# Optimization experiments

Hardware: AMD Instinct MI355X
Metric: run time of the kernel (lower is better)

## Reference

```python
import jax, jax.numpy as jnp
import numpy as np

HEADS = 4
N_NODES = 100000
N_EDGES = 800000
N_LAB = 200000
IN_CH = 64
HID = 32
OUT_CH = 32
EXPR_OUT = 500


def _gat_conv(x, edge_index, W, a_src, a_dst, bias, out_per_head):
    """PyG GATConv, concat=False (mean over heads), eval mode (no dropout)."""
    N = x.shape[0]
    src, dst = edge_index[0], edge_index[1]
    h = (x @ W).reshape(N, HEADS, out_per_head)          # [N,H,C]
    alpha_src = (h * a_src).sum(-1)                       # [N,H]
    alpha_dst = (h * a_dst).sum(-1)                       # [N,H]
    e = jax.nn.leaky_relu(alpha_src[src] + alpha_dst[dst], 0.2)  # [E,H]
    # softmax over incoming edges of each dst node
    m = jax.ops.segment_max(e, dst, num_segments=N)
    ex = jnp.exp(e - m[dst])
    denom = jax.ops.segment_sum(ex, dst, num_segments=N)
    alpha = ex / (denom[dst] + 1e-16)                     # [E,H]
    agg = jax.ops.segment_sum(h[src] * alpha[..., None], dst, num_segments=N)  # [N,H,C]
    return agg.mean(axis=1) + bias                        # [N,C]


def setup_inputs() -> dict:
    key = jax.random.key(0)
    ks = jax.random.split(key, 20)
    g = lambda k, shp, fan: jax.random.normal(k, shp, dtype=jnp.float32) * (1.0 / np.sqrt(fan))
    h2 = HID * 2
    inp = {
        "x": jax.random.normal(ks[0], (N_NODES, IN_CH), dtype=jnp.float32),
        "edge_index": jax.random.randint(ks[1], (2, N_EDGES), 0, N_NODES, dtype=jnp.int64 if jax.config.jax_enable_x64 else jnp.int32),
        "edge_label_index": jax.random.randint(ks[2], (2, N_LAB), 0, N_NODES, dtype=jnp.int64 if jax.config.jax_enable_x64 else jnp.int32),
        # GAT layer 0: in=64 -> out-per-head=hid*2=64, heads=4
        "W0": g(ks[3], (IN_CH, HEADS * h2), IN_CH),
        "as0": g(ks[4], (HEADS, h2), h2),
        "ad0": g(ks[5], (HEADS, h2), h2),
        "b0": jnp.zeros((h2,), dtype=jnp.float32),
        # GAT layer 1: in=hid*2=64 -> out-per-head=hid=32, heads=4
        "W1": g(ks[6], (h2, HEADS * HID), h2),
        "as1": g(ks[7], (HEADS, HID), HID),
        "ad1": g(ks[8], (HEADS, HID), HID),
        "b1": jnp.zeros((HID,), dtype=jnp.float32),
        # lin: hid -> out_channels
        "lin_w": g(ks[9], (HID, OUT_CH), HID),
        "lin_b": jnp.zeros((OUT_CH,), dtype=jnp.float32),
        # expression decoder: out -> hid -> 2*hid -> 3*hid -> expr_out
        "d1_w": g(ks[10], (OUT_CH, HID), OUT_CH),
        "d1_b": jnp.zeros((HID,), dtype=jnp.float32),
        "d2_w": g(ks[11], (HID, 2 * HID), HID),
        "d2_b": jnp.zeros((2 * HID,), dtype=jnp.float32),
        "d3_w": g(ks[12], (2 * HID, 3 * HID), 2 * HID),
        "d3_b": jnp.zeros((3 * HID,), dtype=jnp.float32),
        "d4_w": g(ks[13], (3 * HID, EXPR_OUT), 3 * HID),
        "d4_b": jnp.zeros((EXPR_OUT,), dtype=jnp.float32),
    }
    return inp


def reference(x, edge_index, edge_label_index,
              W0, as0, ad0, b0, W1, as1, ad1, b1,
              lin_w, lin_b, d1_w, d1_b, d2_w, d2_b, d3_w, d3_b, d4_w, d4_b):
    # encode (eval mode: dropout identity)
    h = jax.nn.relu(_gat_conv(x, edge_index, W0, as0, ad0, b0, HID * 2))
    h = jax.nn.relu(_gat_conv(h, edge_index, W1, as1, ad1, b1, HID))
    z = h @ lin_w + lin_b                                  # [N, out]
    # decode_link: inner product per labeled edge
    link = (z[edge_label_index[0]] * z[edge_label_index[1]]).sum(-1)  # [E_lab]
    # decode_expression: 4-layer MLP
    e = jax.nn.relu(z @ d1_w + d1_b)
    e = jax.nn.relu(e @ d2_w + d2_b)
    e = jax.nn.relu(e @ d3_w + d3_b)
    expr = e @ d4_w + d4_b                                 # [N, expr_out]
    return link, expr
```

## Files before the change

kernel.cpp:

```cpp
#include <hip/hip_runtime.h>

#define NN 100000
#define NE 800000
#define NL 200000
#define HEADS 4

template<int K, int TPB, int RPB, bool RELU, bool BIAS>
__launch_bounds__(TPB)
__global__ void gemm_rows(const float* __restrict__ A, const float* __restrict__ B,
                          const float* __restrict__ bias, float* __restrict__ C,
                          int n_rows, int ncols) {
    __shared__ float As[RPB][K];
    const int row0 = blockIdx.x * RPB;
    for (int i = threadIdx.x; i < RPB * K; i += TPB) {
        int r = i / K, k = i % K;
        int gr = row0 + r;
        As[r][k] = (gr < n_rows) ? A[(size_t)gr * K + k] : 0.f;
    }
    __syncthreads();
    const int cpr = TPB / RPB;
    const int r   = threadIdx.x / cpr;
    const int j0  = threadIdx.x % cpr;
    const int gr  = row0 + r;
    if (gr >= n_rows) return;
    for (int j = j0; j < ncols; j += cpr) {
        float s = BIAS ? bias[j] : 0.f;
        #pragma unroll
        for (int k = 0; k < K; ++k) s += As[r][k] * B[k * ncols + j];
        if (RELU) s = fmaxf(s, 0.f);
        C[(size_t)gr * ncols + j] = s;
    }
}

template<int K, int BN, bool RELU, bool BIAS>
__launch_bounds__(256, 4)
__global__ void gemm_tiled(const float* __restrict__ A, const float* __restrict__ B,
                           const float* __restrict__ bias, float* __restrict__ C,
                           int M, int N) {
    constexpr int BM = 64, BK = 32;
    constexpr int TN = BN / 16;
    __shared__ float As[BK][BM];
    __shared__ float Bs[BK][BN];

    const int tid  = threadIdx.x;
    const int row0 = blockIdx.x * BM;
    const int col0 = blockIdx.y * BN;
    const int ty   = tid >> 4;
    const int tx   = tid & 15;

    float acc[4][TN];
    #pragma unroll
    for (int i = 0; i < 4; ++i)
        #pragma unroll
        for (int j = 0; j < TN; ++j) acc[i][j] = 0.f;

    for (int k0 = 0; k0 < K; k0 += BK) {
        for (int i = tid * 4; i < BM * BK; i += 1024) {
            int r  = i >> 5;
            int kk = i & 31;
            int gr = row0 + r;
            float4 v = make_float4(0.f, 0.f, 0.f, 0.f);
            if (gr < M) v = *(const float4*)(A + (size_t)gr * K + k0 + kk);
            int sw = ((kk >> 2) & 3) << 3;
            As[kk + 0][r ^ sw] = v.x;
            As[kk + 1][r ^ sw] = v.y;
            As[kk + 2][r ^ sw] = v.z;
            As[kk + 3][r ^ sw] = v.w;
        }
        for (int i = tid * 4; i < BK * BN; i += 1024) {
            int kk = i / BN, c = i % BN;
            int gc = col0 + c;
            float4 v = make_float4(0.f, 0.f, 0.f, 0.f);
            if (gc < N) v = *(const float4*)(B + (size_t)(k0 + kk) * N + gc);
            *(float4*)&Bs[kk][c] = v;
        }
        __syncthreads();

        #pragma unroll
        for (int kk = 0; kk < BK; ++kk) {
            int sw = ((kk >> 2) & 3) << 3;
            float4 a  = *(const float4*)&As[kk][(ty * 4) ^ sw];
            float4 b0 = *(const float4*)&Bs[kk][tx * 4];
            float av[4] = {a.x, a.y, a.z, a.w};
            float bv[TN];
            bv[0] = b0.x; bv[1] = b0.y; bv[2] = b0.z; bv[3] = b0.w;
            if constexpr (TN == 8) {
                float4 b1 = *(const float4*)&Bs[kk][64 + tx * 4];
                bv[4] = b1.x; bv[5] = b1.y; bv[6] = b1.z; bv[7] = b1.w;
            }
            #pragma unroll
            for (int i = 0; i < 4; ++i)
                #pragma unroll
                for (int j = 0; j < TN; ++j)
                    acc[i][j] = fmaf(av[i], bv[j], acc[i][j]);
        }
        __syncthreads();
    }

    #pragma unroll
    for (int i = 0; i < 4; ++i) {
        int gr = row0 + ty * 4 + i;
        if (gr >= M) continue;
        #pragma unroll
        for (int jh = 0; jh < TN / 4; ++jh) {
            int gc = col0 + jh * 64 + tx * 4;
            if (gc >= N) continue;
            float4 o = make_float4(acc[i][jh * 4 + 0], acc[i][jh * 4 + 1],
                                   acc[i][jh * 4 + 2], acc[i][jh * 4 + 3]);
            if (BIAS) { o.x += bias[gc]; o.y += bias[gc + 1]; o.z += bias[gc + 2]; o.w += bias[gc + 3]; }
            if (RELU) { o.x = fmaxf(o.x, 0.f); o.y = fmaxf(o.y, 0.f); o.z = fmaxf(o.z, 0.f); o.w = fmaxf(o.w, 0.f); }
            *(float4*)(C + (size_t)gr * N + gc) = o;
        }
    }
}

template<int C>
__global__ void calc_alpha(const float* __restrict__ h, const float* __restrict__ a_src,
                           const float* __restrict__ a_dst, float* __restrict__ as_out,
                           float* __restrict__ ad_out) {
    int i = blockIdx.x * blockDim.x + threadIdx.x;
    if (i >= NN * HEADS) return;
    int n = i / HEADS, hd = i % HEADS;
    const float* hp  = h + (size_t)n * HEADS * C + hd * C;
    const float* asp = a_src + hd * C;
    const float* adp = a_dst + hd * C;
    float s1 = 0.f, s2 = 0.f;
    #pragma unroll 8
    for (int c = 0; c < C; ++c) { float v = hp[c]; s1 += v * asp[c]; s2 += v * adp[c]; }
    as_out[i] = s1; ad_out[i] = s2;
}

__device__ __forceinline__ float lrelu02(float v) { return v > 0.f ? v : 0.2f * v; }

__global__ void edge_denom(const int* __restrict__ src, const int* __restrict__ dst,
                           const float* __restrict__ as_, const float* __restrict__ ad_,
                           float* __restrict__ den) {
    int i = blockIdx.x * blockDim.x + threadIdx.x;
    if (i >= NE * HEADS) return;
    int e = i / HEADS, hd = i % HEADS;
    int s = src[e], d = dst[e];
    float v = lrelu02(as_[s * HEADS + hd] + ad_[d * HEADS + hd]);
    atomicAdd(&den[d * HEADS + hd], __expf(v));
}

template<int C>
__global__ void edge_agg(const int* __restrict__ src, const int* __restrict__ dst,
                         const float* __restrict__ as_, const float* __restrict__ ad_,
                         const float* __restrict__ den, const float* __restrict__ h,
                         float* __restrict__ agg) {
    int tid = blockIdx.x * blockDim.x + threadIdx.x;
    int e = tid / C, c = tid % C;
    if (e >= NE) return;
    int s = src[e], d = dst[e];
    float w[HEADS];
    #pragma unroll
    for (int hd = 0; hd < HEADS; ++hd) {
        float v = lrelu02(as_[s * HEADS + hd] + ad_[d * HEADS + hd]);
        w[hd] = __expf(v) / (den[d * HEADS + hd] + 1e-16f);
    }
    float sum = 0.f;
    #pragma unroll
    for (int hd = 0; hd < HEADS; ++hd)
        sum += w[hd] * h[(size_t)s * HEADS * C + hd * C + c];
    atomicAdd(&agg[(size_t)d * C + c], sum);
}

template<int C>
__global__ void finalize(const float* __restrict__ agg, const float* __restrict__ bias,
                         float* __restrict__ out) {
    int i = blockIdx.x * blockDim.x + threadIdx.x;
    if (i >= NN * C) return;
    out[i] = fmaxf(agg[i] * 0.25f + bias[i % C], 0.f);
}

__global__ void link_kernel(const int* __restrict__ lsrc, const int* __restrict__ ldst,
                            const float* __restrict__ z, float* __restrict__ out) {
    int e = blockIdx.x * blockDim.x + threadIdx.x;
    if (e >= NL) return;
    const float4* zs = (const float4*)(z + (size_t)lsrc[e] * 32);
    const float4* zd = (const float4*)(z + (size_t)ldst[e] * 32);
    float sum = 0.f;
    #pragma unroll
    for (int i = 0; i < 8; ++i) {
        float4 a = zs[i], b = zd[i];
        sum += a.x * b.x + a.y * b.y + a.z * b.z + a.w * b.w;
    }
    out[e] = sum;
}

extern "C" void kernel_launch(void* const* d_in, const int* in_sizes, int n_in,
                              void* d_out, int out_size, void* d_ws, size_t ws_size,
                              hipStream_t stream) {
    const float* x     = (const float*)d_in[0];
    const int*   ei    = (const int*)d_in[1];
    const int*   eli   = (const int*)d_in[2];
    const float* W0    = (const float*)d_in[3];
    const float* as0   = (const float*)d_in[4];
    const float* ad0   = (const float*)d_in[5];
    const float* b0    = (const float*)d_in[6];
    const float* W1    = (const float*)d_in[7];
    const float* as1   = (const float*)d_in[8];
    const float* ad1   = (const float*)d_in[9];
    const float* b1    = (const float*)d_in[10];
    const float* lin_w = (const float*)d_in[11];
    const float* lin_b = (const float*)d_in[12];
    const float* d1_w  = (const float*)d_in[13];
    const float* d1_b  = (const float*)d_in[14];
    const float* d2_w  = (const float*)d_in[15];
    const float* d2_b  = (const float*)d_in[16];
    const float* d3_w  = (const float*)d_in[17];
    const float* d3_b  = (const float*)d_in[18];
    const float* d4_w  = (const float*)d_in[19];
    const float* d4_b  = (const float*)d_in[20];

    const int* src = ei;
    const int* dst = ei + NE;
    const int* ls  = eli;
    const int* ld  = eli + NL;

    float* ws = (float*)d_ws;
    float* h_buf = ws;
    float* agg   = ws + (size_t)NN * 256;
    float* outb  = ws + (size_t)NN * 320;
    float* asb   = ws + (size_t)NN * 384;
    float* adb   = ws + (size_t)NN * 388;
    float* den   = ws + (size_t)NN * 392;
    float* z  = h_buf;
    float* e1 = h_buf + (size_t)NN * 32;
    float* e2 = h_buf + (size_t)NN * 64;
    float* e3 = h_buf + (size_t)NN * 128;

    float* link_out = (float*)d_out;
    float* expr_out = (float*)d_out + NL;

    const int GM = (NN + 63) / 64;

    gemm_tiled<64, 128, false, false><<<dim3(GM, 2), 256, 0, stream>>>(x, W0, nullptr, h_buf, NN, 256);
    calc_alpha<64><<<(NN * HEADS + 255) / 256, 256, 0, stream>>>(h_buf, as0, ad0, asb, adb);
    hipMemsetAsync(den, 0, (size_t)NN * HEADS * 4, stream);
    edge_denom<<<(NE * HEADS + 255) / 256, 256, 0, stream>>>(src, dst, asb, adb, den);
    hipMemsetAsync(agg, 0, (size_t)NN * 64 * 4, stream);
    edge_agg<64><<<(size_t)(NE * 64) / 256, 256, 0, stream>>>(src, dst, asb, adb, den, h_buf, agg);
    finalize<64><<<(NN * 64) / 256, 256, 0, stream>>>(agg, b0, outb);

    gemm_tiled<64, 128, false, false><<<dim3(GM, 1), 256, 0, stream>>>(outb, W1, nullptr, h_buf, NN, 128);
    calc_alpha<32><<<(NN * HEADS + 255) / 256, 256, 0, stream>>>(h_buf, as1, ad1, asb, adb);
    hipMemsetAsync(den, 0, (size_t)NN * HEADS * 4, stream);
    edge_denom<<<(NE * HEADS + 255) / 256, 256, 0, stream>>>(src, dst, asb, adb, den);
    hipMemsetAsync(agg, 0, (size_t)NN * 32 * 4, stream);
    edge_agg<32><<<(size_t)(NE * 32) / 256, 256, 0, stream>>>(src, dst, asb, adb, den, h_buf, agg);
    finalize<32><<<(NN * 32) / 256, 256, 0, stream>>>(agg, b1, outb);

    gemm_rows<32, 256, 8, false, true><<<NN / 8, 256, 0, stream>>>(outb, lin_w, lin_b, z, NN, 32);

    link_kernel<<<(NL + 255) / 256, 256, 0, stream>>>(ls, ld, z, link_out);

    gemm_rows<32, 256, 8, true, true><<<NN / 8, 256, 0, stream>>>(z, d1_w, d1_b, e1, NN, 32);
    gemm_tiled<32, 64,  true,  true><<<dim3(GM, 1), 256, 0, stream>>>(e1, d2_w, d2_b, e2, NN, 64);
    gemm_tiled<64, 64,  true,  true><<<dim3(GM, 2), 256, 0, stream>>>(e2, d3_w, d3_b, e3, NN, 96);
    gemm_tiled<96, 128, false, true><<<dim3(GM, 4), 256, 0, stream>>>(e3, d4_w, d4_b, expr_out, NN, 500);
}
```

Measured before the change: 1.326 ms.

## Add larger-tile GEMM kernel and precompute normalized edge attention weights

Adds gemm_tiled2, a 512-thread GEMM with 128-row tiles and up to 256-column tiles. It replaces the tiled GEMMs for the two GAT projections and the last two decoder layers, so fewer blocks are launched and each A tile is reused across more columns. The edge softmax is restructured: edge_denom now stores each exp value, a new edge_weight kernel divides it by the denominator, and edge_agg reads that precomputed weight. This removes the repeated gathers of as/ad/den and the repeated exp in every per-channel thread. In exchange it costs an extra kernel launch and an extra pass that reads and writes an E×H buffer per layer, and it raises register pressure in the wider GEMM tiles.

```diff
diff --git a/kernel.cpp b/kernel.cpp
--- a/kernel.cpp
+++ b/kernel.cpp
@@ -41,18 +41,13 @@
     constexpr int TN = BN / 16;
     __shared__ float As[BK][BM];
     __shared__ float Bs[BK][BN];
-
     const int tid  = threadIdx.x;
     const int row0 = blockIdx.x * BM;
     const int col0 = blockIdx.y * BN;
     const int ty   = tid >> 4;
     const int tx   = tid & 15;
 
-    float acc[4][TN];
-    #pragma unroll
-    for (int i = 0; i < 4; ++i)
-        #pragma unroll
-        for (int j = 0; j < TN; ++j) acc[i][j] = 0.f;
+    float acc[4][TN] = {};
 
     for (int k0 = 0; k0 < K; k0 += BK) {
         for (int i = tid * 4; i < BM * BK; i += 1024) {
@@ -75,18 +70,16 @@
             *(float4*)&Bs[kk][c] = v;
         }
         __syncthreads();
-
         #pragma unroll
         for (int kk = 0; kk < BK; ++kk) {
             int sw = ((kk >> 2) & 3) << 3;
-            float4 a  = *(const float4*)&As[kk][(ty * 4) ^ sw];
-            float4 b0 = *(const float4*)&Bs[kk][tx * 4];
+            float4 a = *(const float4*)&As[kk][(ty * 4) ^ sw];
             float av[4] = {a.x, a.y, a.z, a.w};
             float bv[TN];
-            bv[0] = b0.x; bv[1] = b0.y; bv[2] = b0.z; bv[3] = b0.w;
-            if constexpr (TN == 8) {
-                float4 b1 = *(const float4*)&Bs[kk][64 + tx * 4];
-                bv[4] = b1.x; bv[5] = b1.y; bv[6] = b1.z; bv[7] = b1.w;
+            #pragma unroll
+            for (int q = 0; q < TN / 4; ++q) {
+                float4 b = *(const float4*)&Bs[kk][q * 64 + tx * 4];
+                bv[q*4+0] = b.x; bv[q*4+1] = b.y; bv[q*4+2] = b.z; bv[q*4+3] = b.w;
             }
             #pragma unroll
             for (int i = 0; i < 4; ++i)
@@ -102,13 +95,92 @@
         int gr = row0 + ty * 4 + i;
         if (gr >= M) continue;
         #pragma unroll
-        for (int jh = 0; jh < TN / 4; ++jh) {
-            int gc = col0 + jh * 64 + tx * 4;
+        for (int q = 0; q < TN / 4; ++q) {
+            int gc = col0 + q * 64 + tx * 4;
             if (gc >= N) continue;
-            float4 o = make_float4(acc[i][jh * 4 + 0], acc[i][jh * 4 + 1],
-                                   acc[i][jh * 4 + 2], acc[i][jh * 4 + 3]);
-            if (BIAS) { o.x += bias[gc]; o.y += bias[gc + 1]; o.z += bias[gc + 2]; o.w += bias[gc + 3]; }
-            if (RELU) { o.x = fmaxf(o.x, 0.f); o.y = fmaxf(o.y, 0.f); o.z = fmaxf(o.z, 0.f); o.w = fmaxf(o.w, 0.f); }
+            float4 o = make_float4(acc[i][q*4], acc[i][q*4+1], acc[i][q*4+2], acc[i][q*4+3]);
+            if (BIAS) { o.x += bias[gc]; o.y += bias[gc+1]; o.z += bias[gc+2]; o.w += bias[gc+3]; }
+            if (RELU) { o.x = fmaxf(o.x,0.f); o.y = fmaxf(o.y,0.f); o.z = fmaxf(o.z,0.f); o.w = fmaxf(o.w,0.f); }
+            *(float4*)(C + (size_t)gr * N + gc) = o;
+        }
+    }
+}
+
+template<int K, int BN, bool RELU, bool BIAS>
+__launch_bounds__(512, 4)
+__global__ void gemm_tiled2(const float* __restrict__ A, const float* __restrict__ B,
+                            const float* __restrict__ bias, float* __restrict__ C,
+                            int M, int N) {
+    constexpr int BM = 128, BK = 32;
+    constexpr int TN = BN / 16;
+    __shared__ float As[BK][BM];
+    __shared__ float Bs[BK][BN];
+    const int tid  = threadIdx.x;
+    const int row0 = blockIdx.x * BM;
+    const int col0 = blockIdx.y * BN;
+    const int ty   = tid >> 4;
+    const int tx   = tid & 15;
+
+    float acc[4][TN] = {};
+
+    #pragma unroll 1
+    for (int k0 = 0; k0 < K; k0 += BK) {
+        #pragma unroll
+        for (int i0 = 0; i0 < BM * BK; i0 += 2048) {
+            int i  = i0 + tid * 4;
+            int r  = i >> 5;
+            int kk = i & 31;
+            int gr = row0 + r;
+            float4 v = make_float4(0.f, 0.f, 0.f, 0.f);
+            if (gr < M) v = *(const float4*)(A + (size_t)gr * K + k0 + kk);
+            int sw = ((kk >> 2) & 3) << 3;
+            As[kk + 0][r ^ sw] = v.x;
+            As[kk + 1][r ^ sw] = v.y;
+            As[kk + 2][r ^ sw] = v.z;
+            As[kk + 3][r ^ sw] = v.w;
+        }
+        #pragma unroll
+        for (int i0 = 0; i0 < BK * BN; i0 += 2048) {
+            int i  = i0 + tid * 4;
+            int kk = i / BN, c = i % BN;
+            int gc = col0 + c;
+            float4 v = make_float4(0.f, 0.f, 0.f, 0.f);
+            if (gc < N) v = *(const float4*)(B + (size_t)(k0 + kk) * N + gc);
+            *(float4*)&Bs[kk][c] = v;
+        }
+        __syncthreads();
+
+        #pragma unroll
+        for (int kk = 0; kk < BK; ++kk) {
+            int sw = ((kk >> 2) & 3) << 3;
+            float4 a = *(const float4*)&As[kk][(ty * 4) ^ sw];
+            float av[4] = {a.x, a.y, a.z, a.w};
+            float bv[TN];
+            #pragma unroll
+            for (int q = 0; q < TN / 4; ++q) {
+                float4 b = *(const float4*)&Bs[kk][q * 64 + tx * 4];
+                bv[q*4+0] = b.x; bv[q*4+1] = b.y; bv[q*4+2] = b.z; bv[q*4+3] = b.w;
+            }
+            #pragma unroll
+            for (int i = 0; i < 4; ++i)
+                #pragma unroll
+                for (int j = 0; j < TN; ++j)
+                    acc[i][j] = fmaf(av[i], bv[j], acc[i][j]);
+        }
+        __syncthreads();
+    }
+
+    #pragma unroll
+    for (int i = 0; i < 4; ++i) {
+        int gr = row0 + ty * 4 + i;
+        if (gr >= M) continue;
+        #pragma unroll
+        for (int q = 0; q < TN / 4; ++q) {
+            int gc = col0 + q * 64 + tx * 4;
+            if (gc >= N) continue;
+            float4 o = make_float4(acc[i][q*4], acc[i][q*4+1], acc[i][q*4+2], acc[i][q*4+3]);
+            if (BIAS) { o.x += bias[gc]; o.y += bias[gc+1]; o.z += bias[gc+2]; o.w += bias[gc+3]; }
+            if (RELU) { o.x = fmaxf(o.x,0.f); o.y = fmaxf(o.y,0.f); o.z = fmaxf(o.z,0.f); o.w = fmaxf(o.w,0.f); }
             *(float4*)(C + (size_t)gr * N + gc) = o;
         }
     }
@@ -134,34 +206,38 @@
 
 __global__ void edge_denom(const int* __restrict__ src, const int* __restrict__ dst,
                            const float* __restrict__ as_, const float* __restrict__ ad_,
-                           float* __restrict__ den) {
+                           float* __restrict__ den, float* __restrict__ exb) {
     int i = blockIdx.x * blockDim.x + threadIdx.x;
     if (i >= NE * HEADS) return;
     int e = i / HEADS, hd = i % HEADS;
     int s = src[e], d = dst[e];
     float v = lrelu02(as_[s * HEADS + hd] + ad_[d * HEADS + hd]);
-    atomicAdd(&den[d * HEADS + hd], __expf(v));
+    float ex = __expf(v);
+    exb[i] = ex;
+    atomicAdd(&den[d * HEADS + hd], ex);
+}
+
+__global__ void edge_weight(const int* __restrict__ dst, const float* __restrict__ den,
+                            float* __restrict__ exb) {
+    int i = blockIdx.x * blockDim.x + threadIdx.x;
+    if (i >= NE * HEADS) return;
+    int e = i >> 2, hd = i & 3;
+    int d = dst[e];
+    exb[i] = exb[i] / (den[d * HEADS + hd] + 1e-16f);
 }
 
 template<int C>
 __global__ void edge_agg(const int* __restrict__ src, const int* __restrict__ dst,
-                         const float* __restrict__ as_, const float* __restrict__ ad_,
-                         const float* __restrict__ den, const float* __restrict__ h,
+                         const float* __restrict__ wb, const float* __restrict__ h,
                          float* __restrict__ agg) {
     int tid = blockIdx.x * blockDim.x + threadIdx.x;
     int e = tid / C, c = tid % C;
     if (e >= NE) return;
     int s = src[e], d = dst[e];
-    float w[HEADS];
-    #pragma unroll
-    for (int hd = 0; hd < HEADS; ++hd) {
-        float v = lrelu02(as_[s * HEADS + hd] + ad_[d * HEADS + hd]);
-        w[hd] = __expf(v) / (den[d * HEADS + hd] + 1e-16f);
-    }
     float sum = 0.f;
     #pragma unroll
     for (int hd = 0; hd < HEADS; ++hd)
-        sum += w[hd] * h[(size_t)s * HEADS * C + hd * C + c];
+        sum += wb[e * HEADS + hd] * h[(size_t)s * HEADS * C + hd * C + c];
     atomicAdd(&agg[(size_t)d * C + c], sum);
 }
 
@@ -225,6 +301,7 @@
     float* asb   = ws + (size_t)NN * 384;
     float* adb   = ws + (size_t)NN * 388;
     float* den   = ws + (size_t)NN * 392;
+    float* exb   = ws + (size_t)NN * 396;
     float* z  = h_buf;
     float* e1 = h_buf + (size_t)NN * 32;
     float* e2 = h_buf + (size_t)NN * 64;
@@ -233,22 +310,25 @@
     float* link_out = (float*)d_out;
     float* expr_out = (float*)d_out + NL;
 
-    const int GM = (NN + 63) / 64;
-
-    gemm_tiled<64, 128, false, false><<<dim3(GM, 2), 256, 0, stream>>>(x, W0, nullptr, h_buf, NN, 256);
+    const int GM  = (NN + 63) / 64;
+    const int GM2 = (NN + 127) / 128;
+
+    gemm_tiled2<64, 256, false, false><<<dim3(GM2, 1), 512, 0, stream>>>(x, W0, nullptr, h_buf, NN, 256);
     calc_alpha<64><<<(NN * HEADS + 255) / 256, 256, 0, stream>>>(h_buf, as0, ad0, asb, adb);
     hipMemsetAsync(den, 0, (size_t)NN * HEADS * 4, stream);
-    edge_denom<<<(NE * HEADS + 255) / 256, 256, 0, stream>>>(src, dst, asb, adb, den);
+    edge_denom<<<(NE * HEADS + 255) / 256, 256, 0, stream>>>(src, dst, asb, adb, den, exb);
+    edge_weight<<<(NE * HEADS + 255) / 256, 256, 0, stream>>>(dst, den, exb);
     hipMemsetAsync(agg, 0, (size_t)NN * 64 * 4, stream);
-    edge_agg<64><<<(size_t)(NE * 64) / 256, 256, 0, stream>>>(src, dst, asb, adb, den, h_buf, agg);
+    edge_agg<64><<<(size_t)(NE * 64) / 256, 256, 0, stream>>>(src, dst, exb, h_buf, agg);
     finalize<64><<<(NN * 64) / 256, 256, 0, stream>>>(agg, b0, outb);
 
-    gemm_tiled<64, 128, false, false><<<dim3(GM, 1), 256, 0, stream>>>(outb, W1, nullptr, h_buf, NN, 128);
+    gemm_tiled2<64, 128, false, false><<<dim3(GM2, 1), 512, 0, stream>>>(outb, W1, nullptr, h_buf, NN, 128);
     calc_alpha<32><<<(NN * HEADS + 255) / 256, 256, 0, stream>>>(h_buf, as1, ad1, asb, adb);
     hipMemsetAsync(den, 0, (size_t)NN * HEADS * 4, stream);
-    edge_denom<<<(NE * HEADS + 255) / 256, 256, 0, stream>>>(src, dst, asb, adb, den);
+    edge_denom<<<(NE * HEADS + 255) / 256, 256, 0, stream>>>(src, dst, asb, adb, den, exb);
+    edge_weight<<<(NE * HEADS + 255) / 256, 256, 0, stream>>>(dst, den, exb);
     hipMemsetAsync(agg, 0, (size_t)NN * 32 * 4, stream);
-    edge_agg<32><<<(size_t)(NE * 32) / 256, 256, 0, stream>>>(src, dst, asb, adb, den, h_buf, agg);
+    edge_agg<32><<<(size_t)(NE * 32) / 256, 256, 0, stream>>>(src, dst, exb, h_buf, agg);
     finalize<32><<<(NN * 32) / 256, 256, 0, stream>>>(agg, b1, outb);
 
     gemm_rows<32, 256, 8, false, true><<<NN / 8, 256, 0, stream>>>(outb, lin_w, lin_b, z, NN, 32);
@@ -257,6 +337,6 @@
 
     gemm_rows<32, 256, 8, true, true><<<NN / 8, 256, 0, stream>>>(z, d1_w, d1_b, e1, NN, 32);
     gemm_tiled<32, 64,  true,  true><<<dim3(GM, 1), 256, 0, stream>>>(e1, d2_w, d2_b, e2, NN, 64);
-    gemm_tiled<64, 64,  true,  true><<<dim3(GM, 2), 256, 0, stream>>>(e2, d3_w, d3_b, e3, NN, 96);
-    gemm_tiled<96, 128, false, true><<<dim3(GM, 4), 256, 0, stream>>>(e3, d4_w, d4_b, expr_out, NN, 500);
-}
+    gemm_tiled2<64, 128, true,  true><<<dim3(GM2, 1), 512, 0, stream>>>(e2, d3_w, d3_b, e3, NN, 96);
+    gemm_tiled2<96, 256, false, true><<<dim3(GM2, 2), 512, 0, stream>>>(e3, d4_w, d4_b, expr_out, NN, 500);
+}
```

Result: slower. 1.549 ms (+16.8%).

## Replace atomic edge scatter with CSR-by-destination gather aggregation

Applied to the files above, without the earlier changes.

Builds a CSR grouped by destination on the device each call: a degree histogram, a three-pass scan, then a scatter of source indices. Both GAT layers then use one gather kernel per node. It computes the softmax denominator and the weighted float4 sums in registers, reduces across heads with shuffles, and applies bias, mean and ReLU in the same kernel. This removes the per-edge float atomics, the memsets, and the separate denominator and finalize passes. In exchange it adds CSR construction cost and per-node work that depends on degree. The attention weights are recomputed in two passes over the neighbours.

```diff
diff --git a/kernel.cpp b/kernel.cpp
--- a/kernel.cpp
+++ b/kernel.cpp
@@ -41,18 +41,13 @@
     constexpr int TN = BN / 16;
     __shared__ float As[BK][BM];
     __shared__ float Bs[BK][BN];
-
     const int tid  = threadIdx.x;
     const int row0 = blockIdx.x * BM;
     const int col0 = blockIdx.y * BN;
     const int ty   = tid >> 4;
     const int tx   = tid & 15;
 
-    float acc[4][TN];
-    #pragma unroll
-    for (int i = 0; i < 4; ++i)
-        #pragma unroll
-        for (int j = 0; j < TN; ++j) acc[i][j] = 0.f;
+    float acc[4][TN] = {};
 
     for (int k0 = 0; k0 < K; k0 += BK) {
         for (int i = tid * 4; i < BM * BK; i += 1024) {
@@ -75,18 +70,16 @@
             *(float4*)&Bs[kk][c] = v;
         }
         __syncthreads();
-
         #pragma unroll
         for (int kk = 0; kk < BK; ++kk) {
             int sw = ((kk >> 2) & 3) << 3;
-            float4 a  = *(const float4*)&As[kk][(ty * 4) ^ sw];
-            float4 b0 = *(const float4*)&Bs[kk][tx * 4];
+            float4 a = *(const float4*)&As[kk][(ty * 4) ^ sw];
             float av[4] = {a.x, a.y, a.z, a.w};
             float bv[TN];
-            bv[0] = b0.x; bv[1] = b0.y; bv[2] = b0.z; bv[3] = b0.w;
-            if constexpr (TN == 8) {
-                float4 b1 = *(const float4*)&Bs[kk][64 + tx * 4];
-                bv[4] = b1.x; bv[5] = b1.y; bv[6] = b1.z; bv[7] = b1.w;
+            #pragma unroll
+            for (int q = 0; q < TN / 4; ++q) {
+                float4 b = *(const float4*)&Bs[kk][q * 64 + tx * 4];
+                bv[q*4+0] = b.x; bv[q*4+1] = b.y; bv[q*4+2] = b.z; bv[q*4+3] = b.w;
             }
             #pragma unroll
             for (int i = 0; i < 4; ++i)
@@ -102,13 +95,12 @@
         int gr = row0 + ty * 4 + i;
         if (gr >= M) continue;
         #pragma unroll
-        for (int jh = 0; jh < TN / 4; ++jh) {
-            int gc = col0 + jh * 64 + tx * 4;
+        for (int q = 0; q < TN / 4; ++q) {
+            int gc = col0 + q * 64 + tx * 4;
             if (gc >= N) continue;
-            float4 o = make_float4(acc[i][jh * 4 + 0], acc[i][jh * 4 + 1],
-                                   acc[i][jh * 4 + 2], acc[i][jh * 4 + 3]);
-            if (BIAS) { o.x += bias[gc]; o.y += bias[gc + 1]; o.z += bias[gc + 2]; o.w += bias[gc + 3]; }
-            if (RELU) { o.x = fmaxf(o.x, 0.f); o.y = fmaxf(o.y, 0.f); o.z = fmaxf(o.z, 0.f); o.w = fmaxf(o.w, 0.f); }
+            float4 o = make_float4(acc[i][q*4], acc[i][q*4+1], acc[i][q*4+2], acc[i][q*4+3]);
+            if (BIAS) { o.x += bias[gc]; o.y += bias[gc+1]; o.z += bias[gc+2]; o.w += bias[gc+3]; }
+            if (RELU) { o.x = fmaxf(o.x,0.f); o.y = fmaxf(o.y,0.f); o.z = fmaxf(o.z,0.f); o.w = fmaxf(o.w,0.f); }
             *(float4*)(C + (size_t)gr * N + gc) = o;
         }
     }
@@ -132,45 +124,111 @@
 
 __device__ __forceinline__ float lrelu02(float v) { return v > 0.f ? v : 0.2f * v; }
 
-__global__ void edge_denom(const int* __restrict__ src, const int* __restrict__ dst,
-                           const float* __restrict__ as_, const float* __restrict__ ad_,
-                           float* __restrict__ den) {
-    int i = blockIdx.x * blockDim.x + threadIdx.x;
-    if (i >= NE * HEADS) return;
-    int e = i / HEADS, hd = i % HEADS;
-    int s = src[e], d = dst[e];
-    float v = lrelu02(as_[s * HEADS + hd] + ad_[d * HEADS + hd]);
-    atomicAdd(&den[d * HEADS + hd], __expf(v));
+__global__ void deg_hist(const int* __restrict__ dst, int* __restrict__ deg) {
+    int e = blockIdx.x * blockDim.x + threadIdx.x;
+    if (e < NE) atomicAdd(&deg[dst[e]], 1);
+}
+
+__global__ void scan1(const int* __restrict__ deg, int* __restrict__ rs, int* __restrict__ bsum) {
+    __shared__ int sd[256];
+    int i = blockIdx.x * 256 + threadIdx.x;
+    int v = (i < NN) ? deg[i] : 0;
+    sd[threadIdx.x] = v;
+    __syncthreads();
+    for (int off = 1; off < 256; off <<= 1) {
+        int t = (threadIdx.x >= off) ? sd[threadIdx.x - off] : 0;
+        __syncthreads();
+        sd[threadIdx.x] += t;
+        __syncthreads();
+    }
+    if (i < NN) rs[i] = sd[threadIdx.x] - v;
+    if (threadIdx.x == 255) bsum[blockIdx.x] = sd[255];
+}
+
+__global__ void scan2(int* __restrict__ bsum, int n) {
+    __shared__ int sd[512];
+    int v = (threadIdx.x < n) ? bsum[threadIdx.x] : 0;
+    sd[threadIdx.x] = v;
+    __syncthreads();
+    for (int off = 1; off < 512; off <<= 1) {
+        int t = (threadIdx.x >= off) ? sd[threadIdx.x - off] : 0;
+        __syncthreads();
+        sd[threadIdx.x] += t;
+        __syncthreads();
+    }
+    if (threadIdx.x < n) bsum[threadIdx.x] = sd[threadIdx.x] - v;
+}
+
+__global__ void scan3(int* __restrict__ rs, int* __restrict__ cursor, const int* __restrict__ bsum) {
+    int i = blockIdx.x * 256 + threadIdx.x;
+    if (i < NN) {
+        int v = rs[i] + bsum[blockIdx.x];
+        rs[i] = v;
+        cursor[i] = v;
+    }
+    if (i == 0) rs[NN] = NE;
+}
+
+__global__ void csr_scatter(const int* __restrict__ src, const int* __restrict__ dst,
+                            int* __restrict__ cursor, int* __restrict__ csr_src) {
+    int e = blockIdx.x * blockDim.x + threadIdx.x;
+    if (e < NE) {
+        int pos = atomicAdd(&cursor[dst[e]], 1);
+        csr_src[pos] = src[e];
+    }
 }
 
 template<int C>
-__global__ void edge_agg(const int* __restrict__ src, const int* __restrict__ dst,
-                         const float* __restrict__ as_, const float* __restrict__ ad_,
-                         const float* __restrict__ den, const float* __restrict__ h,
-                         float* __restrict__ agg) {
-    int tid = blockIdx.x * blockDim.x + threadIdx.x;
-    int e = tid / C, c = tid % C;
-    if (e >= NE) return;
-    int s = src[e], d = dst[e];
-    float w[HEADS];
+__launch_bounds__(256)
+__global__ void csr_agg(const int* __restrict__ row_start, const int* __restrict__ csr_src,
+                        const float* __restrict__ as_, const float* __restrict__ ad_,
+                        const float* __restrict__ h, const float* __restrict__ bias,
+                        float* __restrict__ out) {
+    constexpr int NPB = 256 / C;
+    const int tid = threadIdx.x;
+    const int grp = tid / C;
+    const int l   = tid % C;
+    const int hd  = l / (C / 4);
+    const int c4  = (l % (C / 4)) * 4;
+    const int d   = blockIdx.x * NPB + grp;
+    if (d >= NN) return;
+    const int rs = row_start[d], re = row_start[d + 1];
+    const float adv = ad_[d * 4 + hd];
+
+    float den = 0.f;
+    for (int i = rs; i < re; ++i) {
+        int s = csr_src[i];
+        den += __expf(lrelu02(as_[s * 4 + hd] + adv));
+    }
+    const float inv = 1.f / (den + 1e-16f);
+
+    float4 acc = make_float4(0.f, 0.f, 0.f, 0.f);
+    int s = (rs < re) ? csr_src[rs] : 0;
+    for (int i = rs; i < re; ++i) {
+        int sn = (i + 1 < re) ? csr_src[i + 1] : 0;
+        float w = __expf(lrelu02(as_[s * 4 + hd] + adv)) * inv;
+        float4 hv = *(const float4*)(h + (size_t)s * (4 * C) + hd * C + c4);
+        acc.x = fmaf(w, hv.x, acc.x);
+        acc.y = fmaf(w, hv.y, acc.y);
+        acc.z = fmaf(w, hv.z, acc.z);
+        acc.w = fmaf(w, hv.w, acc.w);
+        s = sn;
+    }
     #pragma unroll
-    for (int hd = 0; hd < HEADS; ++hd) {
-        float v = lrelu02(as_[s * HEADS + hd] + ad_[d * HEADS + hd]);
-        w[hd] = __expf(v) / (den[d * HEADS + hd] + 1e-16f);
-    }
-    float sum = 0.f;
-    #pragma unroll
-    for (int hd = 0; hd < HEADS; ++hd)
-        sum += w[hd] * h[(size_t)s * HEADS * C + hd * C + c];
-    atomicAdd(&agg[(size_t)d * C + c], sum);
-}
-
-template<int C>
-__global__ void finalize(const float* __restrict__ agg, const float* __restrict__ bias,
-                         float* __restrict__ out) {
-    int i = blockIdx.x * blockDim.x + threadIdx.x;
-    if (i >= NN * C) return;
-    out[i] = fmaxf(agg[i] * 0.25f + bias[i % C], 0.f);
+    for (int off = C / 4; off < C; off <<= 1) {
+        acc.x += __shfl_xor(acc.x, off);
+        acc.y += __shfl_xor(acc.y, off);
+        acc.z += __shfl_xor(acc.z, off);
+        acc.w += __shfl_xor(acc.w, off);
+    }
+    if (hd == 0) {
+        float4 o;
+        o.x = fmaxf(fmaf(acc.x, 0.25f, bias[c4 + 0]), 0.f);
+        o.y = fmaxf(fmaf(acc.y, 0.25f, bias[c4 + 1]), 0.f);
+        o.z = fmaxf(fmaf(acc.z, 0.25f, bias[c4 + 2]), 0.f);
+        o.w = fmaxf(fmaf(acc.w, 0.25f, bias[c4 + 3]), 0.f);
+        *(float4*)(out + (size_t)d * C + c4) = o;
+    }
 }
 
 __global__ void link_kernel(const int* __restrict__ lsrc, const int* __restrict__ ldst,
@@ -220,11 +278,14 @@
 
     float* ws = (float*)d_ws;
     float* h_buf = ws;
-    float* agg   = ws + (size_t)NN * 256;
-    float* outb  = ws + (size_t)NN * 320;
-    float* asb   = ws + (size_t)NN * 384;
-    float* adb   = ws + (size_t)NN * 388;
-    float* den   = ws + (size_t)NN * 392;
+    float* outb  = ws + (size_t)NN * 256;
+    float* asb   = ws + (size_t)NN * 320;
+    float* adb   = ws + (size_t)NN * 324;
+    int*   ideg  = (int*)(ws + (size_t)NN * 328);
+    int*   irow  = ideg + NN;
+    int*   icur  = irow + NN + 1;
+    int*   ibsum = icur + NN;
+    int*   isrc  = ibsum + 512;
     float* z  = h_buf;
     float* e1 = h_buf + (size_t)NN * 32;
     float* e2 = h_buf + (size_t)NN * 64;
@@ -234,22 +295,22 @@
     float* expr_out = (float*)d_out + NL;
 
     const int GM = (NN + 63) / 64;
+    const int NB = (NN + 255) / 256;
+
+    hipMemsetAsync(ideg, 0, (size_t)NN * 4, stream);
+    deg_hist<<<(NE + 255) / 256, 256, 0, stream>>>(dst, ideg);
+    scan1<<<NB, 256, 0, stream>>>(ideg, irow, ibsum);
+    scan2<<<1, 512, 0, stream>>>(ibsum, NB);
+    scan3<<<NB, 256, 0, stream>>>(irow, icur, ibsum);
+    csr_scatter<<<(NE + 255) / 256, 256, 0, stream>>>(src, dst, icur, isrc);
 
     gemm_tiled<64, 128, false, false><<<dim3(GM, 2), 256, 0, stream>>>(x, W0, nullptr, h_buf, NN, 256);
     calc_alpha<64><<<(NN * HEADS + 255) / 256, 256, 0, stream>>>(h_buf, as0, ad0, asb, adb);
-    hipMemsetAsync(den, 0, (size_t)NN * HEADS * 4, stream);
-    edge_denom<<<(NE * HEADS + 255) / 256, 256, 0, stream>>>(src, dst, asb, adb, den);
-    hipMemsetAsync(agg, 0, (size_t)NN * 64 * 4, stream);
-    edge_agg<64><<<(size_t)(NE * 64) / 256, 256, 0, stream>>>(src, dst, asb, adb, den, h_buf, agg);
-    finalize<64><<<(NN * 64) / 256, 256, 0, stream>>>(agg, b0, outb);
+    csr_agg<64><<<(NN + 3) / 4, 256, 0, stream>>>(irow, isrc, asb, adb, h_buf, b0, outb);
 
     gemm_tiled<64, 128, false, false><<<dim3(GM, 1), 256, 0, stream>>>(outb, W1, nullptr, h_buf, NN, 128);
     calc_alpha<32><<<(NN * HEADS + 255) / 256, 256, 0, stream>>>(h_buf, as1, ad1, asb, adb);
-    hipMemsetAsync(den, 0, (size_t)NN * HEADS * 4, stream);
-    edge_denom<<<(NE * HEADS + 255) / 256, 256, 0, stream>>>(src, dst, asb, adb, den);
-    hipMemsetAsync(agg, 0, (size_t)NN * 32 * 4, stream);
-    edge_agg<32><<<(size_t)(NE * 32) / 256, 256, 0, stream>>>(src, dst, asb, adb, den, h_buf, agg);
-    finalize<32><<<(NN * 32) / 256, 256, 0, stream>>>(agg, b1, outb);
+    csr_agg<32><<<(NN + 7) / 8, 256, 0, stream>>>(irow, isrc, asb, adb, h_buf, b1, outb);
 
     gemm_rows<32, 256, 8, false, true><<<NN / 8, 256, 0, stream>>>(outb, lin_w, lin_b, z, NN, 32);
 
```

Measured after the change: 1.341 ms. About the same (+1.1%).
